# Performance work log

Hardware: AMD Instinct MI355X
Metric: run time of the kernel (lower is better)

Reference implementation:

```python
import jax, jax.numpy as jnp
import numpy as np

N = 100000
E = 1600000
IN_DIM, HIDDEN, OUT_DIM, HEADS = 256, 128, 64, 2
NEG_SLOPE = 0.2


def setup_inputs() -> dict:
    key = jax.random.key(0)
    ks = jax.random.split(key, 10)
    inv = lambda d: 1.0 / np.sqrt(d)
    return {
        "x": jax.random.normal(ks[0], (N, IN_DIM), dtype=jnp.float32),
        "edge_index": jax.random.randint(ks[1], (2, E), 0, N, dtype=jnp.int64),
        "W1": jax.random.normal(ks[2], (IN_DIM, HEADS * HIDDEN), dtype=jnp.float32) * inv(IN_DIM),
        "att_src1": jax.random.normal(ks[3], (HEADS, HIDDEN), dtype=jnp.float32) * inv(HIDDEN),
        "att_dst1": jax.random.normal(ks[4], (HEADS, HIDDEN), dtype=jnp.float32) * inv(HIDDEN),
        "b1": jnp.zeros((HIDDEN,), dtype=jnp.float32),
        "W2": jax.random.normal(ks[5], (HIDDEN, OUT_DIM), dtype=jnp.float32) * inv(HIDDEN),
        "att_src2": jax.random.normal(ks[6], (1, OUT_DIM), dtype=jnp.float32) * inv(OUT_DIM),
        "att_dst2": jax.random.normal(ks[7], (1, OUT_DIM), dtype=jnp.float32) * inv(OUT_DIM),
        "b2": jnp.zeros((OUT_DIM,), dtype=jnp.float32),
    }


def gat_conv(x, W, att_src, att_dst, bias, src, dst, heads, ch):
    # Linear transform: [N, H, C]
    h = (x @ W).reshape(N, heads, ch)
    # Per-node attention logits: [N, H]
    a_s = jnp.einsum("nhc,hc->nh", h, att_src)
    a_d = jnp.einsum("nhc,hc->nh", h, att_dst)
    # Edge-wise scores (self-loops already in src/dst): [E', H]
    e = jax.nn.leaky_relu(a_s[src] + a_d[dst], NEG_SLOPE)
    # Segment softmax over incoming edges of each dst node
    m = jax.ops.segment_max(e, dst, num_segments=N)
    alpha = jnp.exp(e - m[dst])
    denom = jax.ops.segment_sum(alpha, dst, num_segments=N)
    alpha = alpha / denom[dst]
    # Weighted scatter-add aggregation: [N, H, C]
    out = jax.ops.segment_sum(alpha[:, :, None] * h[src], dst, num_segments=N)
    # concat=False -> mean over heads, then bias
    return out.mean(axis=1) + bias


def reference(x, edge_index, W1, att_src1, att_dst1, b1, W2, att_src2, att_dst2, b2):
    # PyG GATConv default: add self-loops
    loop = jnp.arange(N, dtype=edge_index.dtype)
    src = jnp.concatenate([edge_index[0], loop])
    dst = jnp.concatenate([edge_index[1], loop])
    h = gat_conv(x, W1, att_src1, att_dst1, b1, src, dst, HEADS, HIDDEN)
    h = jax.nn.relu(h)  # dropout is identity in eval mode
    out = gat_conv(h, W2, att_src2, att_dst2, b2, src, dst, 1, OUT_DIM)
    return out
```

## Files before the change

### kernel.cpp

```cpp
#include <hip/hip_runtime.h>
#include <hip/hip_bf16.h>
#include <cstdint>
#include <cstddef>

#define IN_D 256
#define HID 128
#define OUT_D 64
#define NSLOPE 0.2f
#define SBCAP 20480

typedef __attribute__((ext_vector_type(8))) short bf16x8;
typedef __attribute__((ext_vector_type(4))) float f32x4;
typedef __attribute__((ext_vector_type(8))) unsigned short u16x8;
typedef unsigned short u16;

static inline int cdiv(long long a, long long b) { return (int)((a + b - 1) / b); }

__device__ __forceinline__ float lrelu(float v) { return v >= 0.f ? v : NSLOPE * v; }
__device__ __forceinline__ int imin(int a, int b) { return a < b ? a : b; }

__device__ __forceinline__ u16 f2bf(float f) {
  unsigned u = __float_as_uint(f);
  return (u16)((u + 0x7FFFu + ((u >> 16) & 1u)) >> 16);
}
__device__ __forceinline__ float bf2f(u16 h) {
  return __uint_as_float((unsigned)h << 16);
}

__global__ void k_prep(const float* __restrict__ W1, u16* __restrict__ WThi,
                       u16* __restrict__ WTlo, const float* __restrict__ W2,
                       u16* __restrict__ W2Thi, u16* __restrict__ W2Tlo) {
  int idx = blockIdx.x * 256 + threadIdx.x;
  if (idx < IN_D * IN_D) {
    int k = idx >> 8, n = idx & 255;
    float f = W1[idx];
    u16 h = f2bf(f);
    WThi[n * IN_D + k] = h;
    WTlo[n * IN_D + k] = f2bf(f - bf2f(h));
  }
  int idx2 = idx - IN_D * IN_D;
  if (idx2 >= 0 && idx2 < HID * OUT_D) {
    int k = idx2 >> 6, n = idx2 & 63;
    float f = W2[idx2];
    u16 h = f2bf(f);
    W2Thi[n * HID + k] = h;
    W2Tlo[n * HID + k] = f2bf(f - bf2f(h));
  }
}

__launch_bounds__(512)
__global__ void k_gemm1sort(const float* __restrict__ x, const u16* __restrict__ WThi,
                            const u16* __restrict__ WTlo,
                            const float* __restrict__ as1, const float* __restrict__ ad1,
                            u16* __restrict__ hb, float* __restrict__ a_s,
                            float* __restrict__ a_d, int N,
                            const int* __restrict__ ei, int E,
                            int* __restrict__ sbCount, int2* __restrict__ st1,
                            int G1, int G2) {
  __shared__ u16 ldsb[2][10240];
  int bid = blockIdx.x;
  int m2 = (G1 < G2 ? G1 : G2) * 2;
  int type, tb;
  if (bid < m2) { type = bid & 1; tb = bid >> 1; }
  else { int ex = bid - m2; type = (G1 > G2) ? 0 : 1; tb = m2 / 2 + ex; }
  int tid = threadIdx.x;

  if (type == 1) {
    int* hist = (int*)&ldsb[0][0];
    int* gb   = hist + 128;
    int* cur  = hist + 256;
    if (tid < 128) hist[tid] = 0;
    __syncthreads();
    int base = tb * 2048 + tid;
    int sv[4], dv[4]; bool vv[4];
    #pragma unroll
    for (int q = 0; q < 4; ++q) {
      int i = base + q * 512;
      vv[q] = i < E;
      int ic = vv[q] ? i : 0;
      sv[q] = ei[ic];
      dv[q] = ei[E + ic];
    }
    #pragma unroll
    for (int q = 0; q < 4; ++q)
      if (vv[q]) atomicAdd(&hist[dv[q] >> 10], 1);
    __syncthreads();
    if (tid < 128) {
      int h = hist[tid];
      gb[tid] = h ? atomicAdd(&sbCount[tid], h) : 0;
      cur[tid] = 0;
    }
    __syncthreads();
    #pragma unroll
    for (int q = 0; q < 4; ++q)
      if (vv[q]) {
        int sb = dv[q] >> 10;
        int r = atomicAdd(&cur[sb], 1);
        int slot = gb[sb] + r;
        if (slot < SBCAP) st1[(size_t)sb * SBCAP + slot] = make_int2(sv[q], dv[q]);
      }
    return;
  }

  int w = tid >> 6, l = tid & 63;
  int l15 = l & 15, l4 = l >> 4;
  int rowbase = tb * 128 + w * 16;
  int row = rowbase + l15;
  int rowc = (row < N) ? row : (N - 1);
  const float* xp = x + (size_t)rowc * IN_D + l4 * 8;

  f32x4 acc[16];
  #pragma unroll
  for (int t = 0; t < 16; ++t) acc[t] = (f32x4){0.f, 0.f, 0.f, 0.f};

  const int ridx = (l15 * 5 + l4) * 8;

  for (int kk = 0; kk < 8; ++kk) {
    __syncthreads();
    #pragma unroll
    for (int it = 0; it < 2; ++it) {
      int c = tid + it * 512;
      int n = c >> 2, ch = c & 3;
      size_t soff = (size_t)n * IN_D + kk * 32 + ch * 8;
      uint4 vh = *(const uint4*)(WThi + soff);
      uint4 vl = *(const uint4*)(WTlo + soff);
      int dsl = (n * 5 + ch) * 8;
      *(uint4*)&ldsb[0][dsl] = vh;
      *(uint4*)&ldsb[1][dsl] = vl;
    }
    __syncthreads();

    f32x4 v0 = *(const f32x4*)(xp + kk * 32);
    f32x4 v1 = *(const f32x4*)(xp + kk * 32 + 4);
    bf16x8 ah, al;
    #pragma unroll
    for (int j = 0; j < 4; ++j) {
      u16 h0 = f2bf(v0[j]);
      ah[j] = (short)h0; al[j] = (short)f2bf(v0[j] - bf2f(h0));
      u16 h1 = f2bf(v1[j]);
      ah[j + 4] = (short)h1; al[j + 4] = (short)f2bf(v1[j] - bf2f(h1));
    }
    #pragma unroll
    for (int t = 0; t < 16; ++t) {
      bf16x8 bh = *(const bf16x8*)&ldsb[0][ridx + t * 640];
      bf16x8 bl = *(const bf16x8*)&ldsb[1][ridx + t * 640];
      acc[t] = __builtin_amdgcn_mfma_f32_16x16x32_bf16(ah, bh, acc[t], 0, 0, 0);
      acc[t] = __builtin_amdgcn_mfma_f32_16x16x32_bf16(al, bh, acc[t], 0, 0, 0);
      acc[t] = __builtin_amdgcn_mfma_f32_16x16x32_bf16(ah, bl, acc[t], 0, 0, 0);
    }
  }

  #pragma unroll
  for (int r = 0; r < 4; ++r) {
    int rr = rowbase + l4 * 4 + r;
    if (rr < N) {
      u16* hp = hb + (size_t)rr * IN_D + l15;
      #pragma unroll
      for (int t = 0; t < 16; ++t) hp[t * 16] = f2bf(acc[t][r]);
    }
  }
  float asv[16], adv[16];
  #pragma unroll
  for (int t = 0; t < 16; ++t) { asv[t] = as1[t * 16 + l15]; adv[t] = ad1[t * 16 + l15]; }
  float ps0[4] = {}, ps1[4] = {}, pd0[4] = {}, pd1[4] = {};
  #pragma unroll
  for (int t = 0; t < 16; ++t) {
    #pragma unroll
    for (int r = 0; r < 4; ++r) {
      float v = acc[t][r];
      if (t < 8) { ps0[r] += v * asv[t]; pd0[r] += v * adv[t]; }
      else       { ps1[r] += v * asv[t]; pd1[r] += v * adv[t]; }
    }
  }
  #pragma unroll
  for (int r = 0; r < 4; ++r) {
    #pragma unroll
    for (int o = 1; o < 16; o <<= 1) {
      ps0[r] += __shfl_xor(ps0[r], o); ps1[r] += __shfl_xor(ps1[r], o);
      pd0[r] += __shfl_xor(pd0[r], o); pd1[r] += __shfl_xor(pd1[r], o);
    }
    int rr = rowbase + l4 * 4 + r;
    if (l15 == 0 && rr < N) {
      a_s[rr * 2] = ps0[r]; a_s[rr * 2 + 1] = ps1[r];
      a_d[rr * 2] = pd0[r]; a_d[rr * 2 + 1] = pd1[r];
    }
  }
}

__launch_bounds__(256)
__global__ void k_sort2(const int* __restrict__ sbCount, const int2* __restrict__ st1,
                        int* __restrict__ ro, int* __restrict__ col, int N) {
  __shared__ int hist2[1024], pref[1024], cur[1024];
  __shared__ int sc[256];
  __shared__ int gbaseS, cntS;
  int tid = threadIdx.x;
  int sb = blockIdx.x;
  int nb0 = sb << 10;
  if (tid == 0) {
    int g = 0;
    for (int b = 0; b < sb; ++b) g += imin(sbCount[b], SBCAP);
    gbaseS = g;
    cntS = imin(sbCount[sb], SBCAP);
  }
  for (int t = tid; t < 1024; t += 256) hist2[t] = 0;
  __syncthreads();
  int gbase = gbaseS, cnt = cntS;
  const int2* sp = st1 + (size_t)sb * SBCAP;
  for (int j = tid; j < cnt; j += 256) atomicAdd(&hist2[sp[j].y - nb0], 1);
  __syncthreads();
  int a0 = hist2[tid * 4], a1 = hist2[tid * 4 + 1],
      a2 = hist2[tid * 4 + 2], a3 = hist2[tid * 4 + 3];
  int s4 = a0 + a1 + a2 + a3;
  sc[tid] = s4; __syncthreads();
  for (int o = 1; o < 256; o <<= 1) {
    int add = (tid >= o) ? sc[tid - o] : 0;
    __syncthreads();
    sc[tid] += add;
    __syncthreads();
  }
  int eb = sc[tid] - s4;
  pref[tid * 4] = eb;
  pref[tid * 4 + 1] = eb + a0;
  pref[tid * 4 + 2] = eb + a0 + a1;
  pref[tid * 4 + 3] = eb + a0 + a1 + a2;
  __syncthreads();
  for (int t = tid; t < 1024; t += 256) {
    cur[t] = pref[t];
    int n = nb0 + t;
    if (n < N) ro[n] = gbase + pref[t];
  }
  if (sb == (int)gridDim.x - 1 && tid == 0) ro[N] = gbase + cnt;
  __syncthreads();
  for (int j = tid; j < cnt; j += 256) {
    int2 e = sp[j];
    int r = atomicAdd(&cur[e.y - nb0], 1);
    col[gbase + r] = e.x;
  }
}

__launch_bounds__(256)
__global__ void k_fagg1g2(const int* __restrict__ ro, const int* __restrict__ col,
                          const float* __restrict__ a_s, const float* __restrict__ a_d,
                          const u16* __restrict__ hb, const float* __restrict__ b1,
                          const u16* __restrict__ W2Thi, const u16* __restrict__ W2Tlo,
                          const float* __restrict__ as2, const float* __restrict__ ad2,
                          u16* __restrict__ h2b, float* __restrict__ a_s2,
                          float* __restrict__ a_d2, int N) {
  __shared__ float rowLds[16][132];
  __shared__ float red[2][16][4];
  int tid = threadIdx.x;
  int wid = tid >> 6, lane = tid & 63;
  int base = blockIdx.x * 16;

  int half = lane >> 5;
  int l5 = lane & 31;
  int head = l5 >> 4;

  for (int rr = 0; rr < 4; ++rr) {
    int ln = wid * 4 + rr;
    int n = base + ln;
    if (n >= N) { if (lane < 16) for (int q = 0; q < 8; ++q) rowLds[ln][lane * 8 + q] = 0.f; continue; }
    int beg = ro[n], end = ro[n + 1];
    float ad0 = a_d[2 * n], ad1 = a_d[2 * n + 1];
    float myAd = head ? ad1 : ad0;

    float sacc = 0.f;
    float accv[8] = {};
    if (half == 0) {
      float2 asn = *(const float2*)&a_s[2 * (size_t)n];
      float wv = __expf(lrelu((head ? asn.y : asn.x) + myAd));
      sacc = wv;
      const u16x8 hv = *(const u16x8*)&hb[(size_t)n * IN_D + l5 * 8];
      #pragma unroll
      for (int q = 0; q < 8; ++q) accv[q] = wv * bf2f(hv[q]);
    }
    #pragma unroll 4
    for (int j = beg; j < end; j += 2) {
      int jj = j + half;
      bool valid = jj < end;
      int sidx = col[valid ? jj : beg];
      float2 asv = *(const float2*)&a_s[2 * (size_t)sidx];
      float e = (head ? asv.y : asv.x) + myAd;
      float wv = __expf(lrelu(e));
      wv = valid ? wv : 0.f;
      sacc += wv;
      const u16x8 hv = *(const u16x8*)&hb[(size_t)sidx * IN_D + l5 * 8];
      #pragma unroll
      for (int q = 0; q < 8; ++q) accv[q] += wv * bf2f(hv[q]);
    }
    sacc += __shfl_xor(sacc, 32);
    float myScale = 0.5f / sacc;
    #pragma unroll
    for (int q = 0; q < 8; ++q) {
      accv[q] *= myScale;
      accv[q] += __shfl_xor(accv[q], 16);
      accv[q] += __shfl_xor(accv[q], 32);
    }
    if (lane < 16) {
      #pragma unroll
      for (int q = 0; q < 8; ++q) rowLds[ln][lane * 8 + q] = accv[q];
    }
  }
  __syncthreads();

  int l15 = lane & 15, l4 = lane >> 4;
  f32x4 acc2 = (f32x4){0.f, 0.f, 0.f, 0.f};
  #pragma unroll
  for (int kk = 0; kk < 4; ++kk) {
    int k0 = kk * 32 + l4 * 8;
    f32x4 bv0 = *(const f32x4*)(b1 + k0);
    f32x4 bv1 = *(const f32x4*)(b1 + k0 + 4);
    bf16x8 ah, al;
    #pragma unroll
    for (int j = 0; j < 4; ++j) {
      float u0 = rowLds[l15][k0 + j] + bv0[j]; u0 = (u0 > 0.f) ? u0 : 0.f;
      u16 h0 = f2bf(u0);
      ah[j] = (short)h0; al[j] = (short)f2bf(u0 - bf2f(h0));
      float u1 = rowLds[l15][k0 + 4 + j] + bv1[j]; u1 = (u1 > 0.f) ? u1 : 0.f;
      u16 h1 = f2bf(u1);
      ah[j + 4] = (short)h1; al[j + 4] = (short)f2bf(u1 - bf2f(h1));
    }
    size_t boff = (size_t)(wid * 16 + l15) * HID + k0;
    bf16x8 bh = *(const bf16x8*)(W2Thi + boff);
    bf16x8 bl = *(const bf16x8*)(W2Tlo + boff);
    acc2 = __builtin_amdgcn_mfma_f32_16x16x32_bf16(ah, bh, acc2, 0, 0, 0);
    acc2 = __builtin_amdgcn_mfma_f32_16x16x32_bf16(al, bh, acc2, 0, 0, 0);
    acc2 = __builtin_amdgcn_mfma_f32_16x16x32_bf16(ah, bl, acc2, 0, 0, 0);
  }

  float asv = as2[wid * 16 + l15], adv = ad2[wid * 16 + l15];
  float ps[4], pd[4];
  #pragma unroll
  for (int r = 0; r < 4; ++r) {
    int n = base + l4 * 4 + r;
    if (n < N) h2b[(size_t)n * OUT_D + wid * 16 + l15] = f2bf(acc2[r]);
    ps[r] = acc2[r] * asv; pd[r] = acc2[r] * adv;
    #pragma unroll
    for (int o = 1; o < 16; o <<= 1) { ps[r] += __shfl_xor(ps[r], o); pd[r] += __shfl_xor(pd[r], o); }
    if (l15 == 0) { red[0][l4 * 4 + r][wid] = ps[r]; red[1][l4 * 4 + r][wid] = pd[r]; }
  }
  __syncthreads();
  if (tid < 32) {
    int ln = tid >> 1, kind = tid & 1;
    int n = base + ln;
    if (n < N) {
      float v = red[kind][ln][0] + red[kind][ln][1] + red[kind][ln][2] + red[kind][ln][3];
      if (kind == 0) a_s2[n] = v; else a_d2[n] = v;
    }
  }
}

__launch_bounds__(256)
__global__ void k_fagg2(const int* __restrict__ ro, const int* __restrict__ col,
                        const float* __restrict__ a_s, const float* __restrict__ a_d,
                        const u16* __restrict__ h2b, const float* __restrict__ b2,
                        float* __restrict__ out, int N) {
  int gid = blockIdx.x * blockDim.x + threadIdx.x;
  int n = gid >> 6, lane = gid & 63;
  if (n >= N) return;
  int beg = ro[n], end = ro[n + 1];
  float ad = a_d[n];

  int g = lane >> 3, l3 = lane & 7;
  float sacc = 0.f;
  float accv[8] = {};
  if (g == 0) {
    float w = __expf(lrelu(a_s[n] + ad));
    sacc = w;
    const u16x8 hv = *(const u16x8*)&h2b[(size_t)n * OUT_D + l3 * 8];
    #pragma unroll
    for (int q = 0; q < 8; ++q) accv[q] = w * bf2f(hv[q]);
  }
  #pragma unroll 4
  for (int j = beg; j < end; j += 8) {
    int jj = j + g;
    bool valid = jj < end;
    int sidx = col[valid ? jj : beg];
    float w = __expf(lrelu(a_s[sidx] + ad));
    w = valid ? w : 0.f;
    sacc += w;
    const u16x8 hv = *(const u16x8*)&h2b[(size_t)sidx * OUT_D + l3 * 8];
    #pragma unroll
    for (int q = 0; q < 8; ++q) accv[q] += w * bf2f(hv[q]);
  }
  sacc += __shfl_xor(sacc, 8);
  sacc += __shfl_xor(sacc, 16);
  sacc += __shfl_xor(sacc, 32);
  float rcp = 1.f / sacc;
  #pragma unroll
  for (int q = 0; q < 8; ++q) {
    accv[q] *= rcp;
    accv[q] += __shfl_xor(accv[q], 8);
    accv[q] += __shfl_xor(accv[q], 16);
    accv[q] += __shfl_xor(accv[q], 32);
  }
  if (lane < 8) {
    float* op = out + (size_t)n * OUT_D + lane * 8;
    const float* bp = b2 + lane * 8;
    float4 o0 = {accv[0] + bp[0], accv[1] + bp[1], accv[2] + bp[2], accv[3] + bp[3]};
    float4 o1 = {accv[4] + bp[4], accv[5] + bp[5], accv[6] + bp[6], accv[7] + bp[7]};
    *(float4*)op = o0;
    *(float4*)(op + 4) = o1;
  }
}

extern "C" void kernel_launch(void* const* d_in, const int* in_sizes, int n_in,
                              void* d_out, int out_size, void* d_ws, size_t ws_size,
                              hipStream_t stream) {
  const float* x    = (const float*)d_in[0];
  const int*   ei   = (const int*)d_in[1];
  const float* W1   = (const float*)d_in[2];
  const float* as1w = (const float*)d_in[3];
  const float* ad1w = (const float*)d_in[4];
  const float* b1   = (const float*)d_in[5];
  const float* W2   = (const float*)d_in[6];
  const float* as2w = (const float*)d_in[7];
  const float* ad2w = (const float*)d_in[8];
  const float* b2   = (const float*)d_in[9];
  float* out = (float*)d_out;

  const int N   = in_sizes[0] / IN_D;
  const int E   = in_sizes[1] / 2;
  const int NSB = cdiv(N, 1024);

  float* ws = (float*)d_ws;
  size_t off = 0;
  u16*   hb1  = (u16*)(ws + off); off += (size_t)N * IN_D / 2;
  u16*   h2b  = (u16*)(ws + off); off += (size_t)N * OUT_D / 2;
  float* a_s1 = ws + off; off += (size_t)N * 2;
  float* a_d1 = ws + off; off += (size_t)N * 2;
  float* a_s2 = ws + off; off += N;
  float* a_d2 = ws + off; off += N;
  int*   sbCount = (int*)(ws + off); off += 128;
  int2*  st1  = (int2*)(ws + off); off += (size_t)NSB * SBCAP * 2;
  int*   ro   = (int*)(ws + off); off += (size_t)N + 1;
  int*   col  = (int*)(ws + off); off += E;
  u16*   WThi = (u16*)(ws + off); off += (IN_D * IN_D) / 2;
  u16*   WTlo = (u16*)(ws + off); off += (IN_D * IN_D) / 2;
  u16*   W2Thi = (u16*)(ws + off); off += (HID * OUT_D) / 2;
  u16*   W2Tlo = (u16*)(ws + off); off += (HID * OUT_D) / 2;

  hipMemsetAsync(sbCount, 0, 128 * sizeof(int), stream);

  k_prep<<<cdiv(IN_D * IN_D + HID * OUT_D, 256), 256, 0, stream>>>(
      W1, WThi, WTlo, W2, W2Thi, W2Tlo);

  const int G1 = cdiv(N, 128);
  const int G2 = cdiv(E, 2048);
  k_gemm1sort<<<G1 + G2, 512, 0, stream>>>(x, WThi, WTlo, as1w, ad1w, hb1, a_s1, a_d1, N,
                                           ei, E, sbCount, st1, G1, G2);

  k_sort2<<<NSB, 256, 0, stream>>>(sbCount, st1, ro, col, N);

  k_fagg1g2<<<cdiv(N, 16), 256, 0, stream>>>(ro, col, a_s1, a_d1, hb1, b1,
                                             W2Thi, W2Tlo, as2w, ad2w, h2b, a_s2, a_d2, N);

  k_fagg2<<<cdiv((long long)N * 64, 256), 256, 0, stream>>>(ro, col, a_s2, a_d2, h2b, b2, out, N);
}
```

Measured before the change: 369.4 us.

## Rebalance kernel fusion: merge prep with sort pass 1, GEMM with sort pass 2

The weight prep/bf16 split now shares a launch with the first bucketing pass of edge sorting. The second CSR sort pass (per-superbucket histogram, scan, scatter) runs as extra blocks inside the GEMM1 kernel. This removes one kernel launch and hides sort pass 2 behind the GEMM instead of running it serially. The cost is heavier sort2 blocks sharing the 512-thread, large-LDS GEMM configuration and a longer 512-wide scan.

New measurement: 301.5 us. -18.4%, faster.

```diff
diff --git a/kernel.cpp b/kernel.cpp
--- a/kernel.cpp
+++ b/kernel.cpp
@@ -27,36 +27,82 @@
   return __uint_as_float((unsigned)h << 16);
 }
 
-__global__ void k_prep(const float* __restrict__ W1, u16* __restrict__ WThi,
-                       u16* __restrict__ WTlo, const float* __restrict__ W2,
-                       u16* __restrict__ W2Thi, u16* __restrict__ W2Tlo) {
-  int idx = blockIdx.x * 256 + threadIdx.x;
-  if (idx < IN_D * IN_D) {
-    int k = idx >> 8, n = idx & 255;
-    float f = W1[idx];
-    u16 h = f2bf(f);
-    WThi[n * IN_D + k] = h;
-    WTlo[n * IN_D + k] = f2bf(f - bf2f(h));
-  }
-  int idx2 = idx - IN_D * IN_D;
-  if (idx2 >= 0 && idx2 < HID * OUT_D) {
-    int k = idx2 >> 6, n = idx2 & 63;
-    float f = W2[idx2];
-    u16 h = f2bf(f);
-    W2Thi[n * HID + k] = h;
-    W2Tlo[n * HID + k] = f2bf(f - bf2f(h));
-  }
-}
-
-__launch_bounds__(512)
-__global__ void k_gemm1sort(const float* __restrict__ x, const u16* __restrict__ WThi,
-                            const u16* __restrict__ WTlo,
-                            const float* __restrict__ as1, const float* __restrict__ ad1,
-                            u16* __restrict__ hb, float* __restrict__ a_s,
-                            float* __restrict__ a_d, int N,
+__launch_bounds__(256)
+__global__ void k_prepsort1(const float* __restrict__ W1, u16* __restrict__ WThi,
+                            u16* __restrict__ WTlo, const float* __restrict__ W2,
+                            u16* __restrict__ W2Thi, u16* __restrict__ W2Tlo,
                             const int* __restrict__ ei, int E,
                             int* __restrict__ sbCount, int2* __restrict__ st1,
-                            int G1, int G2) {
+                            int GP, int GS) {
+  __shared__ int hist[128], gb[128], cur[128];
+  int bid = blockIdx.x;
+  int m2 = (GP < GS ? GP : GS) * 2;
+  int type, tb;
+  if (bid < m2) { type = bid & 1; tb = bid >> 1; }
+  else { int ex = bid - m2; type = (GP > GS) ? 0 : 1; tb = m2 / 2 + ex; }
+  int tid = threadIdx.x;
+
+  if (type == 0) {
+    int idx = tb * 256 + tid;
+    if (idx < IN_D * IN_D) {
+      int k = idx >> 8, n = idx & 255;
+      float f = W1[idx];
+      u16 h = f2bf(f);
+      WThi[n * IN_D + k] = h;
+      WTlo[n * IN_D + k] = f2bf(f - bf2f(h));
+    }
+    int idx2 = idx - IN_D * IN_D;
+    if (idx2 >= 0 && idx2 < HID * OUT_D) {
+      int k = idx2 >> 6, n = idx2 & 63;
+      float f = W2[idx2];
+      u16 h = f2bf(f);
+      W2Thi[n * HID + k] = h;
+      W2Tlo[n * HID + k] = f2bf(f - bf2f(h));
+    }
+    return;
+  }
+
+  if (tid < 128) hist[tid] = 0;
+  __syncthreads();
+  int base = tb * 2048 + tid;
+  int sv[8], dv[8]; bool vv[8];
+  #pragma unroll
+  for (int q = 0; q < 8; ++q) {
+    int i = base + q * 256;
+    vv[q] = i < E;
+    int ic = vv[q] ? i : 0;
+    sv[q] = ei[ic];
+    dv[q] = ei[E + ic];
+  }
+  #pragma unroll
+  for (int q = 0; q < 8; ++q)
+    if (vv[q]) atomicAdd(&hist[dv[q] >> 10], 1);
+  __syncthreads();
+  if (tid < 128) {
+    int h = hist[tid];
+    gb[tid] = h ? atomicAdd(&sbCount[tid], h) : 0;
+    cur[tid] = 0;
+  }
+  __syncthreads();
+  #pragma unroll
+  for (int q = 0; q < 8; ++q)
+    if (vv[q]) {
+      int sb = dv[q] >> 10;
+      int r = atomicAdd(&cur[sb], 1);
+      int slot = gb[sb] + r;
+      if (slot < SBCAP) st1[(size_t)sb * SBCAP + slot] = make_int2(sv[q], dv[q]);
+    }
+}
+
+__launch_bounds__(512)
+__global__ void k_gemm1sort2(const float* __restrict__ x, const u16* __restrict__ WThi,
+                             const u16* __restrict__ WTlo,
+                             const float* __restrict__ as1, const float* __restrict__ ad1,
+                             u16* __restrict__ hb, float* __restrict__ a_s,
+                             float* __restrict__ a_d, int N,
+                             const int* __restrict__ sbCount, const int2* __restrict__ st1,
+                             int* __restrict__ ro, int* __restrict__ col,
+                             int G1, int G2) {
   __shared__ u16 ldsb[2][10240];
   int bid = blockIdx.x;
   int m2 = (G1 < G2 ? G1 : G2) * 2;
@@ -66,39 +112,50 @@
   int tid = threadIdx.x;
 
   if (type == 1) {
-    int* hist = (int*)&ldsb[0][0];
-    int* gb   = hist + 128;
-    int* cur  = hist + 256;
-    if (tid < 128) hist[tid] = 0;
-    __syncthreads();
-    int base = tb * 2048 + tid;
-    int sv[4], dv[4]; bool vv[4];
-    #pragma unroll
-    for (int q = 0; q < 4; ++q) {
-      int i = base + q * 512;
-      vv[q] = i < E;
-      int ic = vv[q] ? i : 0;
-      sv[q] = ei[ic];
-      dv[q] = ei[E + ic];
-    }
-    #pragma unroll
-    for (int q = 0; q < 4; ++q)
-      if (vv[q]) atomicAdd(&hist[dv[q] >> 10], 1);
-    __syncthreads();
-    if (tid < 128) {
-      int h = hist[tid];
-      gb[tid] = h ? atomicAdd(&sbCount[tid], h) : 0;
-      cur[tid] = 0;
-    }
-    __syncthreads();
-    #pragma unroll
-    for (int q = 0; q < 4; ++q)
-      if (vv[q]) {
-        int sb = dv[q] >> 10;
-        int r = atomicAdd(&cur[sb], 1);
-        int slot = gb[sb] + r;
-        if (slot < SBCAP) st1[(size_t)sb * SBCAP + slot] = make_int2(sv[q], dv[q]);
-      }
+    int* hist2 = (int*)&ldsb[0][0];
+    int* pref  = hist2 + 1024;
+    int* cur   = hist2 + 2048;
+    int* sc    = hist2 + 3072;
+    int* gbc   = hist2 + 3584;
+    int sb = tb;
+    int nb0 = sb << 10;
+    if (tid == 0) {
+      int g = 0;
+      for (int b = 0; b < sb; ++b) g += imin(sbCount[b], SBCAP);
+      gbc[0] = g;
+      gbc[1] = imin(sbCount[sb], SBCAP);
+    }
+    for (int t = tid; t < 1024; t += 512) hist2[t] = 0;
+    __syncthreads();
+    int gbase = gbc[0], cnt = gbc[1];
+    const int2* sp = st1 + (size_t)sb * SBCAP;
+    for (int j = tid; j < cnt; j += 512) atomicAdd(&hist2[sp[j].y - nb0], 1);
+    __syncthreads();
+    int a0 = hist2[tid * 2], a1 = hist2[tid * 2 + 1];
+    int s2 = a0 + a1;
+    sc[tid] = s2; __syncthreads();
+    for (int o = 1; o < 512; o <<= 1) {
+      int add = (tid >= o) ? sc[tid - o] : 0;
+      __syncthreads();
+      sc[tid] += add;
+      __syncthreads();
+    }
+    int eb = sc[tid] - s2;
+    pref[tid * 2] = eb;
+    pref[tid * 2 + 1] = eb + a0;
+    __syncthreads();
+    for (int t = tid; t < 1024; t += 512) {
+      cur[t] = pref[t];
+      int n = nb0 + t;
+      if (n < N) ro[n] = gbase + pref[t];
+    }
+    if (sb == G2 - 1 && tid == 0) ro[N] = gbase + cnt;
+    __syncthreads();
+    for (int j = tid; j < cnt; j += 512) {
+      int2 e = sp[j];
+      int r = atomicAdd(&cur[e.y - nb0], 1);
+      col[gbase + r] = e.x;
+    }
     return;
   }
 
@@ -184,57 +241,6 @@
       a_s[rr * 2] = ps0[r]; a_s[rr * 2 + 1] = ps1[r];
       a_d[rr * 2] = pd0[r]; a_d[rr * 2 + 1] = pd1[r];
     }
-  }
-}
-
-__launch_bounds__(256)
-__global__ void k_sort2(const int* __restrict__ sbCount, const int2* __restrict__ st1,
-                        int* __restrict__ ro, int* __restrict__ col, int N) {
-  __shared__ int hist2[1024], pref[1024], cur[1024];
-  __shared__ int sc[256];
-  __shared__ int gbaseS, cntS;
-  int tid = threadIdx.x;
-  int sb = blockIdx.x;
-  int nb0 = sb << 10;
-  if (tid == 0) {
-    int g = 0;
-    for (int b = 0; b < sb; ++b) g += imin(sbCount[b], SBCAP);
-    gbaseS = g;
-    cntS = imin(sbCount[sb], SBCAP);
-  }
-  for (int t = tid; t < 1024; t += 256) hist2[t] = 0;
-  __syncthreads();
-  int gbase = gbaseS, cnt = cntS;
-  const int2* sp = st1 + (size_t)sb * SBCAP;
-  for (int j = tid; j < cnt; j += 256) atomicAdd(&hist2[sp[j].y - nb0], 1);
-  __syncthreads();
-  int a0 = hist2[tid * 4], a1 = hist2[tid * 4 + 1],
-      a2 = hist2[tid * 4 + 2], a3 = hist2[tid * 4 + 3];
-  int s4 = a0 + a1 + a2 + a3;
-  sc[tid] = s4; __syncthreads();
-  for (int o = 1; o < 256; o <<= 1) {
-    int add = (tid >= o) ? sc[tid - o] : 0;
-    __syncthreads();
-    sc[tid] += add;
-    __syncthreads();
-  }
-  int eb = sc[tid] - s4;
-  pref[tid * 4] = eb;
-  pref[tid * 4 + 1] = eb + a0;
-  pref[tid * 4 + 2] = eb + a0 + a1;
-  pref[tid * 4 + 3] = eb + a0 + a1 + a2;
-  __syncthreads();
-  for (int t = tid; t < 1024; t += 256) {
-    cur[t] = pref[t];
-    int n = nb0 + t;
-    if (n < N) ro[n] = gbase + pref[t];
-  }
-  if (sb == (int)gridDim.x - 1 && tid == 0) ro[N] = gbase + cnt;
-  __syncthreads();
-  for (int j = tid; j < cnt; j += 256) {
-    int2 e = sp[j];
-    int r = atomicAdd(&cur[e.y - nb0], 1);
-    col[gbase + r] = e.x;
   }
 }
 
@@ -442,15 +448,14 @@
 
   hipMemsetAsync(sbCount, 0, 128 * sizeof(int), stream);
 
-  k_prep<<<cdiv(IN_D * IN_D + HID * OUT_D, 256), 256, 0, stream>>>(
-      W1, WThi, WTlo, W2, W2Thi, W2Tlo);
+  const int GP = cdiv(IN_D * IN_D + HID * OUT_D, 256);
+  const int GS = cdiv(E, 2048);
+  k_prepsort1<<<GP + GS, 256, 0, stream>>>(W1, WThi, WTlo, W2, W2Thi, W2Tlo,
+                                           ei, E, sbCount, st1, GP, GS);
 
   const int G1 = cdiv(N, 128);
-  const int G2 = cdiv(E, 2048);
-  k_gemm1sort<<<G1 + G2, 512, 0, stream>>>(x, WThi, WTlo, as1w, ad1w, hb1, a_s1, a_d1, N,
-                                           ei, E, sbCount, st1, G1, G2);
-
-  k_sort2<<<NSB, 256, 0, stream>>>(sbCount, st1, ro, col, N);
+  k_gemm1sort2<<<G1 + NSB, 512, 0, stream>>>(x, WThi, WTlo, as1w, ad1w, hb1, a_s1, a_d1, N,
+                                             sbCount, st1, ro, col, G1, NSB);
 
   k_fagg1g2<<<cdiv(N, 16), 256, 0, stream>>>(ro, col, a_s1, a_d1, hb1, b1,
                                              W2Thi, W2Tlo, as2w, ad2w, h2b, a_s2, a_d2, N);
```
